# Performance work log

Measured on AMD Instinct MI355X. Metric: run time of the kernel, lower is better.

Reference implementation:

```python
import jax, jax.numpy as jnp
import numpy as np

HIDDEN = 2048
HEADS = 16
HEAD_DIM = HIDDEN // HEADS
ROPE_BASE = 10000.0


def rope_cos_sin(seq_len, dim, dtype=jnp.float32):
    inv_freq = 1.0 / (ROPE_BASE ** (jnp.arange(0, dim, 2, dtype=jnp.float32) / dim))
    t = jnp.arange(seq_len, dtype=jnp.float32)
    freqs = jnp.einsum('i,j->ij', t, inv_freq)            # [S, dim/2]
    emb = jnp.concatenate([freqs, freqs], axis=-1)        # [S, dim]
    return jnp.cos(emb).astype(dtype), jnp.sin(emb).astype(dtype)


def rotate_half(x):
    x1, x2 = jnp.split(x, 2, axis=-1)
    return jnp.concatenate([-x2, x1], axis=-1)


def setup_inputs() -> dict:
    key = jax.random.key(0)
    ks = jax.random.split(key, 6)
    B, S, D = 2, 2048, HIDDEN
    scale = 1.0 / np.sqrt(D)
    x = jax.random.normal(ks[0], (B, S, D), dtype=jnp.float32)
    Wq = jax.random.normal(ks[1], (D, D), dtype=jnp.float32) * scale
    Wk = jax.random.normal(ks[2], (D, D), dtype=jnp.float32) * scale
    Wv = jax.random.normal(ks[3], (D, D), dtype=jnp.float32) * scale
    Wo = jax.random.normal(ks[4], (D, D), dtype=jnp.float32) * scale
    bo = jnp.zeros((D,), dtype=jnp.float32)
    return {"x": x, "Wq": Wq, "Wk": Wk, "Wv": Wv, "Wo": Wo, "bo": bo}


def reference(x, Wq, Wk, Wv, Wo, bo):
    B, S, D = x.shape
    H, Dh = HEADS, HEAD_DIM
    # torch Linear: x @ W.T
    q = (x @ Wq.T).reshape(B, S, H, Dh).transpose(0, 2, 1, 3)  # [B,H,S,Dh]
    k = (x @ Wk.T).reshape(B, S, H, Dh).transpose(0, 2, 1, 3)
    v = (x @ Wv.T).reshape(B, S, H, Dh).transpose(0, 2, 1, 3)
    cos, sin = rope_cos_sin(S, Dh, x.dtype)                    # [S, Dh]
    q = q * cos + rotate_half(q) * sin
    k = k * cos + rotate_half(k) * sin
    scale = Dh ** -0.5
    attn = jnp.einsum('bhqd,bhkd->bhqk', q, k) * scale
    attn = jax.nn.softmax(attn, axis=-1)
    out = jnp.einsum('bhqk,bhkd->bhqd', attn, v)               # [B,H,S,Dh]
    out = out.transpose(0, 2, 1, 3).reshape(B, S, D)
    return out @ Wo.T + bo
```

## Files before the change

kernel.cpp:

```cpp
#include <hip/hip_runtime.h>
#include <stdint.h>


#define SEQ 2048
#define HD 128
#define DMODEL 2048

typedef __bf16 bf16x8 __attribute__((ext_vector_type(8)));
typedef float f32x4 __attribute__((ext_vector_type(4)));
typedef unsigned short u16;
typedef unsigned int u32;

typedef bf16x8 __attribute__((may_alias)) bf16x8_a;
typedef uint2 __attribute__((may_alias)) uint2_a;
typedef uint4 __attribute__((may_alias)) uint4_a;

__device__ __forceinline__ u16 f2bf(float f) {
  unsigned int u = __float_as_uint(f);
  u += 0x7fff + ((u >> 16) & 1);
  return (u16)(u >> 16);
}

typedef __attribute__((address_space(1))) void* gas_t;
typedef __attribute__((address_space(3))) void* las_t;
__device__ __forceinline__ void load_lds16(const void* g, void* l) {
  __builtin_amdgcn_global_load_lds((gas_t)(uintptr_t)g,
                                   (las_t)(uint32_t)(uintptr_t)l, 16, 0, 0);
}

__global__ void conv_all(const float* __restrict__ x,
                         const float* __restrict__ wq,
                         const float* __restrict__ wk,
                         const float* __restrict__ wv,
                         const float* __restrict__ wo,
                         u16* __restrict__ xb, u16* __restrict__ wqkv,
                         u16* __restrict__ wob) {
  int i = blockIdx.x * 256 + threadIdx.x;
  const float* src;
  u16* dst;
  int off;
  if (i < 2097152) { src = x; dst = xb; off = i; }
  else if (i < 3145728) { src = wq; dst = wqkv; off = i - 2097152; }
  else if (i < 4194304) { src = wk; dst = wqkv + 4194304; off = i - 3145728; }
  else if (i < 5242880) { src = wv; dst = wqkv + 8388608; off = i - 4194304; }
  else { src = wo; dst = wob; off = i - 5242880; }
  float4 v = ((const float4*)src)[off];
  ushort4 o;
  o.x = f2bf(v.x); o.y = f2bf(v.y); o.z = f2bf(v.z); o.w = f2bf(v.w);
  ((ushort4*)dst)[off] = o;
}


#define BARR asm volatile("s_barrier" ::: "memory")
#define LGKM0 asm volatile("s_waitcnt lgkmcnt(0)" ::: "memory")
#define VMW6 asm volatile("s_waitcnt vmcnt(6)" ::: "memory")
#define VMW8 asm volatile("s_waitcnt vmcnt(8)" ::: "memory")
#define VMW0 asm volatile("s_waitcnt vmcnt(0)" ::: "memory")

#define STGA(D, KOFF) do {                                                  \
    const u16* ga_ = Ag + (KOFF);                                           \
    u16* la_ = S + (D) * 16384;                                             \
    load_lds16(ga_ + off[0], la_ + tid * 8);                                \
    load_lds16(ga_ + off[1], la_ + (tid + 512) * 8);                        \
    load_lds16(ga_ + off[2], la_ + (tid + 1024) * 8);                       \
    load_lds16(ga_ + off[3], la_ + (tid + 1536) * 8);                       \
  } while (0)

#define STGB(D, KOFF) do {                                                  \
    const u16* gb_ = Bg + (KOFF);                                           \
    u16* lb_ = S + 49152 + (D) * 8192;                                      \
    load_lds16(gb_ + off[0], lb_ + tid * 8);                                \
    load_lds16(gb_ + off[1], lb_ + (tid + 512) * 8);                        \
  } while (0)

#define LDA2(D, MH) do {                                                    \
    const u16* ab_ = S + (D) * 16384;                                       \
    _Pragma("unroll") for (int mt_ = 0; mt_ < 2; ++mt_) {                   \
      int rA_ = wm * 64 + ((MH) * 2 + mt_) * 16 + l15;                      \
      int sw_ = rA_ & 7;                                                    \
      af[mt_][0] = *(const bf16x8_a*)(ab_ + (rA_ * 8 + (quad ^ sw_)) * 8);  \
      af[mt_][1] = *(const bf16x8_a*)(ab_ + (rA_ * 8 + ((4 + quad) ^ sw_)) * 8); \
    } } while (0)

#define LDB2(D) do {                                                        \
    const u16* bb_ = S + 49152 + (D) * 8192;                                \
    _Pragma("unroll") for (int nt_ = 0; nt_ < 4; ++nt_) {                   \
      int rB_ = wn * 64 + nt_ * 16 + l15;                                   \
      int sw_ = rB_ & 7;                                                    \
      bfr[nt_][0] = *(const bf16x8_a*)(bb_ + (rB_ * 8 + (quad ^ sw_)) * 8); \
      bfr[nt_][1] = *(const bf16x8_a*)(bb_ + (rB_ * 8 + ((4 + quad) ^ sw_)) * 8); \
    } } while (0)

#define MM2(MH) do {                                                        \
    __builtin_amdgcn_s_setprio(1);                                          \
    _Pragma("unroll") for (int c_ = 0; c_ < 2; ++c_)                        \
      _Pragma("unroll") for (int mt_ = 0; mt_ < 2; ++mt_)                   \
        _Pragma("unroll") for (int nt_ = 0; nt_ < 4; ++nt_) {               \
          if (VM)                                                           \
            acc[(MH) * 2 + mt_][nt_] =                                      \
                __builtin_amdgcn_mfma_f32_16x16x32_bf16(                    \
                    bfr[nt_][c_], af[mt_][c_],                              \
                    acc[(MH) * 2 + mt_][nt_], 0, 0, 0);                     \
          else                                                              \
            acc[(MH) * 2 + mt_][nt_] =                                      \
                __builtin_amdgcn_mfma_f32_16x16x32_bf16(                    \
                    af[mt_][c_], bfr[nt_][c_],                              \
                    acc[(MH) * 2 + mt_][nt_], 0, 0, 0);                     \
        }                                                                   \
    __builtin_amdgcn_s_setprio(0);                                          \
  } while (0)

#define STEP3(T, CUR, NX2) do {                                             \
    LDA2(CUR, 0); LDB2(CUR);                                                \
    STGA(NX2, ((T) + 2) * 64);                                              \
    BARR; LGKM0; MM2(0); BARR;                                              \
    LDA2(CUR, 1);                                                           \
    STGB(NX2, ((T) + 2) * 64);                                              \
    BARR; LGKM0; MM2(1); VMW6; BARR;                                        \
  } while (0)

template <bool VM>
__device__ __forceinline__ void mm_core(const u16* __restrict__ Ag,
                                        const u16* __restrict__ Bg,
                                        u16* __restrict__ S, int tid,
                                        f32x4 acc[4][4]) {
  const int lane = tid & 63;
  const int wave = tid >> 6;
  const int quad = lane >> 4;
  const int l15 = lane & 15;
  const int wm = wave >> 1;
  const int wn = wave & 1;

  u32 off[4];
#pragma unroll
  for (int j = 0; j < 4; ++j) {
    int idx = tid + j * 512;
    int r = idx >> 3;
    off[j] = (u32)r * 2048u + (u32)(((idx & 7) ^ (r & 7)) * 8);
  }

  bf16x8 af[2][2], bfr[4][2];

  STGA(0, 0);
  STGB(0, 0);
  STGA(1, 64);
  STGB(1, 64);
  VMW6;
  BARR;

#pragma unroll 1
  for (int tt = 0; tt < 30; tt += 3) {
    STEP3(tt,     0, 2);
    STEP3(tt + 1, 1, 0);
    STEP3(tt + 2, 2, 1);
  }

  LDA2(0, 0); LDB2(0);
  BARR; LGKM0; MM2(0); BARR;
  LDA2(0, 1);
  BARR; LGKM0; MM2(1); VMW0; BARR;
  LDA2(1, 0); LDB2(1);
  BARR; LGKM0; MM2(0); BARR;
  LDA2(1, 1);
  BARR; LGKM0; MM2(1); BARR;
}

__global__ __launch_bounds__(512, 2)
void gemm_qkv(const u16* __restrict__ A, const u16* __restrict__ Bm,
              u16* __restrict__ qkv, u16* __restrict__ vt) {
  __shared__ __align__(16) u16 S[73728];

  const int tid = threadIdx.x;
  int hwid = blockIdx.y * 48 + blockIdx.x;
  int logical = (hwid & 7) * 96 + (hwid >> 3);
  const int bx = logical >> 4;
  const int by = logical & 15;
  const int row0 = by * 256;
  const int col0 = bx * 128;
  const bool vmode = bx >= 32;

  const u16* Ag = A + (size_t)row0 * 2048;
  const u16* Bg = Bm + (size_t)col0 * 2048;

  f32x4 acc[4][4] = {};
  if (vmode) mm_core<true>(Ag, Bg, S, tid, acc);
  else       mm_core<false>(Ag, Bg, S, tid, acc);

  const int lane = tid & 63;
  const int wave = tid >> 6;
  const int quad = lane >> 4;
  const int l15 = lane & 15;
  const int wm = wave >> 1;
  const int wn = wave & 1;

  const int which = bx >> 4;
  const int h = bx & 15;
  const int brow = row0 >> 11;
  const int sbase = row0 & 2047;
  const float qs = (which == 0) ? 0.12751744f : 1.0f;

#pragma unroll
  for (int mt = 0; mt < 4; ++mt)
#pragma unroll
    for (int nt = 0; nt < 4; ++nt)
#pragma unroll
      for (int r = 0; r < 4; ++r) {
        int el;
        if (vmode) {
          int dd = wn * 64 + nt * 16 + quad * 4 + r;
          int ss = wm * 64 + mt * 16 + l15;
          el = dd * 256 + (((ss >> 3) ^ (dd & 31)) * 8) + (ss & 7);
        } else {
          int ss = wm * 64 + mt * 16 + quad * 4 + r;
          int dd = wn * 64 + nt * 16 + l15;
          el = ss * 128 + (((dd >> 3) ^ (ss & 15)) * 8) + (dd & 7);
        }
        S[el] = f2bf(acc[mt][nt][r] * qs);
      }
  __syncthreads();

  if (!vmode) {
    const int a = lane & 7;
    const int sg = lane >> 3;
    const float c1 = 0.2076205059304601f;
    const float c2 = 2.6514961294723187f;
#pragma unroll
    for (int pass = 0; pass < 4; ++pass) {
      int s_l = pass * 64 + wave * 8 + sg;
      int s2048 = sbase + s_l;
      int sw = s_l & 15;
      bf16x8 x1 = *(const bf16x8_a*)&S[s_l * 128 + ((a ^ sw) * 8)];
      bf16x8 x2 = *(const bf16x8_a*)&S[s_l * 128 + (((a + 8) ^ sw) * 8)];
      u16 o1[8], o2[8];
#pragma unroll
      for (int e = 0; e < 8; ++e) {
        float j = (float)(a * 8 + e);
        float rev = (float)s2048 * __builtin_amdgcn_exp2f(-c1 * j - c2);
        rev = __builtin_amdgcn_fractf(rev);
        float sn = __builtin_amdgcn_sinf(rev);
        float cs = __builtin_amdgcn_cosf(rev);
        float v1 = (float)x1[e], v2 = (float)x2[e];
        o1[e] = f2bf(v1 * cs - v2 * sn);
        o2[e] = f2bf(v2 * cs + v1 * sn);
      }
      size_t base =
          ((((size_t)which * 2 + brow) * 16 + h) * SEQ + s2048) * HD + a * 8;
      *(uint4_a*)&qkv[base] = *(uint4*)o1;
      *(uint4_a*)&qkv[base + 64] = *(uint4*)o2;
    }
  } else {
    const int d_part = tid >> 4;
    const int a0 = tid & 15;
#pragma unroll
    for (int pass = 0; pass < 4; ++pass) {
      int d_l = pass * 32 + d_part;
      int dw = d_l & 31;
      size_t rb = (((size_t)brow * 16 + h) * HD + d_l) * SEQ + sbase;
#pragma unroll
      for (int g = 0; g < 2; ++g) {
        int a2 = a0 + g * 16;
        bf16x8 y = *(const bf16x8_a*)&S[d_l * 256 + ((a2 ^ dw) * 8)];
        *(uint4_a*)&vt[rb + a2 * 8] = *(uint4_a*)&y;
      }
    }
  }
}

__global__ __launch_bounds__(512, 2)
void gemm_out(const u16* __restrict__ A, const u16* __restrict__ Bm,
              float* __restrict__ C, const float* __restrict__ bias) {
  __shared__ __align__(16) u16 S[73728];

  const int tid = threadIdx.x;
  int hwid = blockIdx.y * 16 + blockIdx.x;
  int logical = (hwid & 7) * 32 + (hwid >> 3);
  const int bx = logical >> 4;
  const int by = logical & 15;
  const int row0 = by * 256;
  const int col0 = bx * 128;

  const u16* Ag = A + (size_t)row0 * 2048;
  const u16* Bg = Bm + (size_t)col0 * 2048;

  f32x4 acc[4][4] = {};
  mm_core<false>(Ag, Bg, S, tid, acc);

  const int lane = tid & 63;
  const int wave = tid >> 6;
  const int quad = lane >> 4;
  const int l15 = lane & 15;
  const int wm = wave >> 1;
  const int wn = wave & 1;

#pragma unroll
  for (int nt = 0; nt < 4; ++nt) {
    int d = col0 + wn * 64 + nt * 16 + l15;
    float bv = bias[d];
#pragma unroll
    for (int mt = 0; mt < 4; ++mt) {
#pragma unroll
      for (int r = 0; r < 4; ++r) {
        int row = row0 + wm * 64 + mt * 16 + quad * 4 + r;
        C[(size_t)row * DMODEL + d] = acc[mt][nt][r] + bv;
      }
    }
  }
}

__global__ __launch_bounds__(256, 2)
void attn_kernel(const u16* __restrict__ qkv, const u16* __restrict__ vt,
                 u16* __restrict__ attn_out) {
  __shared__ __align__(16) u16 Kl[2][64 * 128];
  __shared__ __align__(16) u16 Vl[2][128 * 64];
  __shared__ __align__(16) u16 Pl[4][32 * 64];

  const int tid = threadIdx.x;
  const int lane = tid & 63;
  const int wave = tid >> 6;
  const int quad = lane >> 4;
  const int l15 = lane & 15;
  const int q0 = blockIdx.x * 128;
  const int bh = blockIdx.y;
  const size_t SD = (size_t)SEQ * HD;

  const u16* Q = qkv + (size_t)bh * SD;
  const u16* Kg = qkv + (size_t)(32 + bh) * SD;
  const u16* Vg = vt + (size_t)bh * SD;

  bf16x8 onesf;
#pragma unroll
  for (int e = 0; e < 8; ++e)
    onesf[e] = (l15 == 0) ? (__bf16)1.0f : (__bf16)0.0f;

  bf16x8 qf[2][4];
#pragma unroll
  for (int mt = 0; mt < 2; ++mt) {
    int qrow = q0 + wave * 32 + mt * 16 + l15;
#pragma unroll
    for (int c = 0; c < 4; ++c)
      qf[mt][c] = *(const bf16x8*)(Q + (size_t)qrow * HD + c * 32 + quad * 8);
  }

  f32x4 of[9][2] = {};
  u16* pw = &Pl[wave][0];

  auto stage = [&](int tile, int buf) {
    int kv0 = tile * 64;
#pragma unroll
    for (int j = 0; j < 4; ++j) {
      int idx = (wave * 4 + j) * 64 + lane;
      {
        int r = idx >> 4, cs = idx & 15;
        int cc = cs ^ (r & 15);
        load_lds16(Kg + (size_t)(kv0 + r) * HD + cc * 8, &Kl[buf][idx * 8]);
      }
      {
        int r = idx >> 3, cs = idx & 7;
        int cc = cs ^ (r & 7);
        load_lds16(Vg + (size_t)r * SEQ + kv0 + cc * 8, &Vl[buf][idx * 8]);
      }
    }
  };

  stage(0, 0);
  stage(1, 1);
  VMW8;
  BARR;

#pragma unroll 2
  for (int t = 0; t < 32; ++t) {
    const u16* Kb = Kl[t & 1];
    const u16* Vb = Vl[t & 1];

    f32x4 sc[4][2] = {};
    __builtin_amdgcn_s_setprio(1);
#pragma unroll
    for (int c = 0; c < 4; ++c) {
      bf16x8 kf[4];
#pragma unroll
      for (int nt = 0; nt < 4; ++nt)
        kf[nt] = *(const bf16x8*)&Kb[((nt * 16 + l15) * 16 +
                                      ((c * 4 + quad) ^ l15)) * 8];
#pragma unroll
      for (int nt = 0; nt < 4; ++nt)
#pragma unroll
        for (int mt = 0; mt < 2; ++mt)
          sc[nt][mt] = __builtin_amdgcn_mfma_f32_16x16x32_bf16(
              kf[nt], qf[mt][c], sc[nt][mt], 0, 0, 0);
    }
    __builtin_amdgcn_s_setprio(0);

#pragma unroll
    for (int nt = 0; nt < 4; ++nt) {
#pragma unroll
      for (int mt = 0; mt < 2; ++mt) {
        float p0 = __builtin_amdgcn_exp2f(sc[nt][mt][0]);
        float p1 = __builtin_amdgcn_exp2f(sc[nt][mt][1]);
        float p2 = __builtin_amdgcn_exp2f(sc[nt][mt][2]);
        float p3 = __builtin_amdgcn_exp2f(sc[nt][mt][3]);
        u32 lo = __builtin_amdgcn_perm(__float_as_uint(p1),
                                       __float_as_uint(p0), 0x07060302u);
        u32 hi = __builtin_amdgcn_perm(__float_as_uint(p3),
                                       __float_as_uint(p2), 0x07060302u);
        int row = mt * 16 + l15;
        int a = nt * 2 + (quad >> 1);
        int idx16 = (row * 8 + (a ^ (l15 & 7))) * 8 + (quad & 1) * 4;
        uint2 pk; pk.x = lo; pk.y = hi;
        *(uint2_a*)&pw[idx16] = pk;
      }
    }

    __builtin_amdgcn_s_setprio(1);
#pragma unroll
    for (int c = 0; c < 2; ++c) {
      bf16x8 pf[2];
#pragma unroll
      for (int mt = 0; mt < 2; ++mt)
        pf[mt] = *(const bf16x8_a*)&pw[((mt * 16 + l15) * 8 +
                                        ((c * 4 + quad) ^ (l15 & 7))) * 8];
#pragma unroll
      for (int dt = 0; dt < 9; ++dt) {
        bf16x8 vf = (dt < 8)
                        ? *(const bf16x8*)&Vb[((dt * 16 + l15) * 8 +
                                               ((c * 4 + quad) ^ (l15 & 7))) * 8]
                        : onesf;
#pragma unroll
        for (int mt = 0; mt < 2; ++mt)
          of[dt][mt] = __builtin_amdgcn_mfma_f32_16x16x32_bf16(
              vf, pf[mt], of[dt][mt], 0, 0, 0);
      }
    }
    __builtin_amdgcn_s_setprio(0);

    BARR;
    if (t < 30) {
      stage(t + 2, t & 1);
      VMW8;
    } else {
      VMW0;
    }
    BARR;
  }

  const int b = bh >> 4, h = bh & 15;
#pragma unroll
  for (int mt = 0; mt < 2; ++mt) {
    float lsum = __shfl(of[8][mt][0], l15, 64);
    float inv = 1.f / lsum;
    int s = q0 + wave * 32 + mt * 16 + l15;
    size_t rowb = ((size_t)b * SEQ + s) * DMODEL + h * HD;
#pragma unroll
    for (int dt = 0; dt < 8; ++dt) {
      ushort4 ov;
      ov.x = f2bf(of[dt][mt][0] * inv);
      ov.y = f2bf(of[dt][mt][1] * inv);
      ov.z = f2bf(of[dt][mt][2] * inv);
      ov.w = f2bf(of[dt][mt][3] * inv);
      *(ushort4*)&attn_out[rowb + dt * 16 + quad * 4] = ov;
    }
  }
}

extern "C" void kernel_launch(void* const* d_in, const int* in_sizes, int n_in,
                              void* d_out, int out_size, void* d_ws,
                              size_t ws_size, hipStream_t stream) {
  const float* x = (const float*)d_in[0];
  const float* Wq = (const float*)d_in[1];
  const float* Wk = (const float*)d_in[2];
  const float* Wv = (const float*)d_in[3];
  const float* Wo = (const float*)d_in[4];
  const float* bo = (const float*)d_in[5];
  float* out = (float*)d_out;

  char* ws = (char*)d_ws;
  u16* xb = (u16*)(ws);
  u16* wqkv = (u16*)(ws + (size_t)(16 << 20));
  u16* wob = (u16*)(ws + (size_t)(40 << 20));
  u16* qkv = (u16*)(ws + (size_t)(48 << 20));
  u16* vt = qkv + (size_t)2 * 8388608;
  u16* attn = xb;

  conv_all<<<24576, 256, 0, stream>>>(x, Wq, Wk, Wv, Wo, xb, wqkv, wob);

  gemm_qkv<<<dim3(48, 16), 512, 0, stream>>>(xb, wqkv, qkv, vt);
  attn_kernel<<<dim3(16, 32), 256, 0, stream>>>(qkv, vt, attn);
  gemm_out<<<dim3(16, 16), 512, 0, stream>>>(attn, wob, out, bo);
}
```

Measured before the change: 356.5 us.

## Remove intra-step barriers in GEMM core, coalesce output stores, batch conversion work

Removes the extra s_barrier and lgkmcnt waits around each MFMA half-step in the shared GEMM core, keeping only the per-step vmcnt wait and barrier that protect the async LDS staging. The output GEMM epilogue now adds bias in registers and stages the tile through LDS so rows are written with coalesced float4 stores. The fp32-to-bf16 conversion kernel processes four chunks per thread with a quarter of the grid. Dropping barriers relies on compiler-inserted waits for LDS reads and could expose races if buffer reuse assumptions are wrong.

After: 376.8 us. 5.7% more time.

```diff
diff --git a/kernel.cpp b/kernel.cpp
--- a/kernel.cpp
+++ b/kernel.cpp
@@ -14,6 +14,7 @@
 typedef bf16x8 __attribute__((may_alias)) bf16x8_a;
 typedef uint2 __attribute__((may_alias)) uint2_a;
 typedef uint4 __attribute__((may_alias)) uint4_a;
+typedef float4 __attribute__((may_alias)) float4_a;
 
 __device__ __forceinline__ u16 f2bf(float f) {
   unsigned int u = __float_as_uint(f);
@@ -35,24 +36,27 @@
                          const float* __restrict__ wo,
                          u16* __restrict__ xb, u16* __restrict__ wqkv,
                          u16* __restrict__ wob) {
-  int i = blockIdx.x * 256 + threadIdx.x;
-  const float* src;
-  u16* dst;
-  int off;
-  if (i < 2097152) { src = x; dst = xb; off = i; }
-  else if (i < 3145728) { src = wq; dst = wqkv; off = i - 2097152; }
-  else if (i < 4194304) { src = wk; dst = wqkv + 4194304; off = i - 3145728; }
-  else if (i < 5242880) { src = wv; dst = wqkv + 8388608; off = i - 4194304; }
-  else { src = wo; dst = wob; off = i - 5242880; }
-  float4 v = ((const float4*)src)[off];
-  ushort4 o;
-  o.x = f2bf(v.x); o.y = f2bf(v.y); o.z = f2bf(v.z); o.w = f2bf(v.w);
-  ((ushort4*)dst)[off] = o;
+  int base = blockIdx.x * 256 + threadIdx.x;
+#pragma unroll
+  for (int rep = 0; rep < 4; ++rep) {
+    int i = base + rep * 1572864;
+    const float* src;
+    u16* dst;
+    int off;
+    if (i < 2097152) { src = x; dst = xb; off = i; }
+    else if (i < 3145728) { src = wq; dst = wqkv; off = i - 2097152; }
+    else if (i < 4194304) { src = wk; dst = wqkv + 4194304; off = i - 3145728; }
+    else if (i < 5242880) { src = wv; dst = wqkv + 8388608; off = i - 4194304; }
+    else { src = wo; dst = wob; off = i - 5242880; }
+    float4 v = ((const float4*)src)[off];
+    ushort4 o;
+    o.x = f2bf(v.x); o.y = f2bf(v.y); o.z = f2bf(v.z); o.w = f2bf(v.w);
+    ((ushort4*)dst)[off] = o;
+  }
 }
 
 
 #define BARR asm volatile("s_barrier" ::: "memory")
-#define LGKM0 asm volatile("s_waitcnt lgkmcnt(0)" ::: "memory")
 #define VMW6 asm volatile("s_waitcnt vmcnt(6)" ::: "memory")
 #define VMW8 asm volatile("s_waitcnt vmcnt(8)" ::: "memory")
 #define VMW0 asm volatile("s_waitcnt vmcnt(0)" ::: "memory")
@@ -113,10 +117,11 @@
 #define STEP3(T, CUR, NX2) do {                                             \
     LDA2(CUR, 0); LDB2(CUR);                                                \
     STGA(NX2, ((T) + 2) * 64);                                              \
-    BARR; LGKM0; MM2(0); BARR;                                              \
+    MM2(0);                                                                 \
     LDA2(CUR, 1);                                                           \
     STGB(NX2, ((T) + 2) * 64);                                              \
-    BARR; LGKM0; MM2(1); VMW6; BARR;                                        \
+    MM2(1);                                                                 \
+    VMW6; BARR;                                                             \
   } while (0)
 
 template <bool VM>
@@ -156,13 +161,15 @@
   }
 
   LDA2(0, 0); LDB2(0);
-  BARR; LGKM0; MM2(0); BARR;
+  MM2(0);
   LDA2(0, 1);
-  BARR; LGKM0; MM2(1); VMW0; BARR;
+  MM2(1);
+  VMW0; BARR;
   LDA2(1, 0); LDB2(1);
-  BARR; LGKM0; MM2(0); BARR;
+  MM2(0);
   LDA2(1, 1);
-  BARR; LGKM0; MM2(1); BARR;
+  MM2(1);
+  BARR;
 }
 
 __global__ __launch_bounds__(512, 2)
@@ -294,16 +301,39 @@
 
 #pragma unroll
   for (int nt = 0; nt < 4; ++nt) {
-    int d = col0 + wn * 64 + nt * 16 + l15;
-    float bv = bias[d];
-#pragma unroll
-    for (int mt = 0; mt < 4; ++mt) {
-#pragma unroll
-      for (int r = 0; r < 4; ++r) {
-        int row = row0 + wm * 64 + mt * 16 + quad * 4 + r;
-        C[(size_t)row * DMODEL + d] = acc[mt][nt][r] + bv;
-      }
-    }
+    float bv = bias[col0 + wn * 64 + nt * 16 + l15];
+#pragma unroll
+    for (int mt = 0; mt < 4; ++mt)
+#pragma unroll
+      for (int r = 0; r < 4; ++r) acc[mt][nt][r] += bv;
+  }
+
+  float* Sf = (float*)S;
+  const int lr = tid >> 2;
+  const int c16 = (tid & 3) << 5;
+#pragma unroll
+  for (int hh = 0; hh < 2; ++hh) {
+    if ((wm >> 1) == hh) {
+      int lrow0 = (wm & 1) * 64;
+#pragma unroll
+      for (int mt = 0; mt < 4; ++mt)
+#pragma unroll
+        for (int nt = 0; nt < 4; ++nt)
+#pragma unroll
+          for (int r = 0; r < 4; ++r) {
+            int lrow = lrow0 + mt * 16 + quad * 4 + r;
+            int col = wn * 64 + nt * 16 + l15;
+            Sf[lrow * 132 + col] = acc[mt][nt][r];
+          }
+    }
+    __syncthreads();
+#pragma unroll
+    for (int k = 0; k < 8; ++k) {
+      float4 v = *(const float4_a*)&Sf[lr * 132 + c16 + k * 4];
+      *(float4_a*)&C[(size_t)(row0 + hh * 128 + lr) * DMODEL + col0 + c16 +
+                     k * 4] = v;
+    }
+    __syncthreads();
   }
 }
 
@@ -480,7 +510,7 @@
   u16* vt = qkv + (size_t)2 * 8388608;
   u16* attn = xb;
 
-  conv_all<<<24576, 256, 0, stream>>>(x, Wq, Wk, Wv, Wo, xb, wqkv, wob);
+  conv_all<<<6144, 256, 0, stream>>>(x, Wq, Wk, Wv, Wo, xb, wqkv, wob);
 
   gemm_qkv<<<dim3(48, 16), 512, 0, stream>>>(xb, wqkv, qkv, vt);
   attn_kernel<<<dim3(16, 32), 256, 0, stream>>>(qkv, vt, attn);
```

## Split attention work over 8 waves and drop redundant GEMM barriers

Applied to the files above, without the earlier changes.

The attention kernel now runs 512 threads per block, with each of the 8 waves owning 16 query rows instead of 32. This halves per-wave accumulators and registers and raises wave-level parallelism, at the cost of each wave reading K/V fragments from LDS for fewer rows. Separately, the GEMM main loop drops the extra s_barrier and lgkmcnt(0) waits around each MFMA half-step. It relies on the compiler's own waits and on multi-buffered staging to keep LDS reads safe, which reduces synchronisation stalls.

Measured after the change: 367.2 us. 1.03x slower.

```diff
diff --git a/kernel.cpp b/kernel.cpp
--- a/kernel.cpp
+++ b/kernel.cpp
@@ -52,9 +52,8 @@
 
 
 #define BARR asm volatile("s_barrier" ::: "memory")
-#define LGKM0 asm volatile("s_waitcnt lgkmcnt(0)" ::: "memory")
 #define VMW6 asm volatile("s_waitcnt vmcnt(6)" ::: "memory")
-#define VMW8 asm volatile("s_waitcnt vmcnt(8)" ::: "memory")
+#define VMW4 asm volatile("s_waitcnt vmcnt(4)" ::: "memory")
 #define VMW0 asm volatile("s_waitcnt vmcnt(0)" ::: "memory")
 
 #define STGA(D, KOFF) do {                                                  \
@@ -113,10 +112,11 @@
 #define STEP3(T, CUR, NX2) do {                                             \
     LDA2(CUR, 0); LDB2(CUR);                                                \
     STGA(NX2, ((T) + 2) * 64);                                              \
-    BARR; LGKM0; MM2(0); BARR;                                              \
+    MM2(0);                                                                 \
     LDA2(CUR, 1);                                                           \
     STGB(NX2, ((T) + 2) * 64);                                              \
-    BARR; LGKM0; MM2(1); VMW6; BARR;                                        \
+    MM2(1);                                                                 \
+    VMW6; BARR;                                                             \
   } while (0)
 
 template <bool VM>
@@ -156,13 +156,15 @@
   }
 
   LDA2(0, 0); LDB2(0);
-  BARR; LGKM0; MM2(0); BARR;
+  MM2(0);
   LDA2(0, 1);
-  BARR; LGKM0; MM2(1); VMW0; BARR;
+  MM2(1);
+  VMW0; BARR;
   LDA2(1, 0); LDB2(1);
-  BARR; LGKM0; MM2(0); BARR;
+  MM2(0);
   LDA2(1, 1);
-  BARR; LGKM0; MM2(1); BARR;
+  MM2(1);
+  BARR;
 }
 
 __global__ __launch_bounds__(512, 2)
@@ -307,12 +309,12 @@
   }
 }
 
-__global__ __launch_bounds__(256, 2)
+__global__ __launch_bounds__(512, 4)
 void attn_kernel(const u16* __restrict__ qkv, const u16* __restrict__ vt,
                  u16* __restrict__ attn_out) {
   __shared__ __align__(16) u16 Kl[2][64 * 128];
   __shared__ __align__(16) u16 Vl[2][128 * 64];
-  __shared__ __align__(16) u16 Pl[4][32 * 64];
+  __shared__ __align__(16) u16 Pl[8][16 * 64];
 
   const int tid = threadIdx.x;
   const int lane = tid & 63;
@@ -332,23 +334,22 @@
   for (int e = 0; e < 8; ++e)
     onesf[e] = (l15 == 0) ? (__bf16)1.0f : (__bf16)0.0f;
 
-  bf16x8 qf[2][4];
-#pragma unroll
-  for (int mt = 0; mt < 2; ++mt) {
-    int qrow = q0 + wave * 32 + mt * 16 + l15;
+  bf16x8 qf[4];
+  {
+    int qrow = q0 + wave * 16 + l15;
 #pragma unroll
     for (int c = 0; c < 4; ++c)
-      qf[mt][c] = *(const bf16x8*)(Q + (size_t)qrow * HD + c * 32 + quad * 8);
-  }
-
-  f32x4 of[9][2] = {};
+      qf[c] = *(const bf16x8*)(Q + (size_t)qrow * HD + c * 32 + quad * 8);
+  }
+
+  f32x4 of[9] = {};
   u16* pw = &Pl[wave][0];
 
   auto stage = [&](int tile, int buf) {
     int kv0 = tile * 64;
 #pragma unroll
-    for (int j = 0; j < 4; ++j) {
-      int idx = (wave * 4 + j) * 64 + lane;
+    for (int j = 0; j < 2; ++j) {
+      int idx = (wave * 2 + j) * 64 + lane;
       {
         int r = idx >> 4, cs = idx & 15;
         int cc = cs ^ (r & 15);
@@ -364,7 +365,7 @@
 
   stage(0, 0);
   stage(1, 1);
-  VMW8;
+  VMW4;
   BARR;
 
 #pragma unroll 2
@@ -372,7 +373,7 @@
     const u16* Kb = Kl[t & 1];
     const u16* Vb = Vl[t & 1];
 
-    f32x4 sc[4][2] = {};
+    f32x4 sc[4] = {};
     __builtin_amdgcn_s_setprio(1);
 #pragma unroll
     for (int c = 0; c < 4; ++c) {
@@ -383,51 +384,40 @@
                                       ((c * 4 + quad) ^ l15)) * 8];
 #pragma unroll
       for (int nt = 0; nt < 4; ++nt)
-#pragma unroll
-        for (int mt = 0; mt < 2; ++mt)
-          sc[nt][mt] = __builtin_amdgcn_mfma_f32_16x16x32_bf16(
-              kf[nt], qf[mt][c], sc[nt][mt], 0, 0, 0);
+        sc[nt] = __builtin_amdgcn_mfma_f32_16x16x32_bf16(
+            kf[nt], qf[c], sc[nt], 0, 0, 0);
     }
     __builtin_amdgcn_s_setprio(0);
 
 #pragma unroll
     for (int nt = 0; nt < 4; ++nt) {
-#pragma unroll
-      for (int mt = 0; mt < 2; ++mt) {
-        float p0 = __builtin_amdgcn_exp2f(sc[nt][mt][0]);
-        float p1 = __builtin_amdgcn_exp2f(sc[nt][mt][1]);
-        float p2 = __builtin_amdgcn_exp2f(sc[nt][mt][2]);
-        float p3 = __builtin_amdgcn_exp2f(sc[nt][mt][3]);
-        u32 lo = __builtin_amdgcn_perm(__float_as_uint(p1),
-                                       __float_as_uint(p0), 0x07060302u);
-        u32 hi = __builtin_amdgcn_perm(__float_as_uint(p3),
-                                       __float_as_uint(p2), 0x07060302u);
-        int row = mt * 16 + l15;
-        int a = nt * 2 + (quad >> 1);
-        int idx16 = (row * 8 + (a ^ (l15 & 7))) * 8 + (quad & 1) * 4;
-        uint2 pk; pk.x = lo; pk.y = hi;
-        *(uint2_a*)&pw[idx16] = pk;
-      }
+      float p0 = __builtin_amdgcn_exp2f(sc[nt][0]);
+      float p1 = __builtin_amdgcn_exp2f(sc[nt][1]);
+      float p2 = __builtin_amdgcn_exp2f(sc[nt][2]);
+      float p3 = __builtin_amdgcn_exp2f(sc[nt][3]);
+      u32 lo = __builtin_amdgcn_perm(__float_as_uint(p1),
+                                     __float_as_uint(p0), 0x07060302u);
+      u32 hi = __builtin_amdgcn_perm(__float_as_uint(p3),
+                                     __float_as_uint(p2), 0x07060302u);
+      int a = nt * 2 + (quad >> 1);
+      int idx16 = (l15 * 8 + (a ^ (l15 & 7))) * 8 + (quad & 1) * 4;
+      uint2 pk; pk.x = lo; pk.y = hi;
+      *(uint2_a*)&pw[idx16] = pk;
     }
 
     __builtin_amdgcn_s_setprio(1);
 #pragma unroll
     for (int c = 0; c < 2; ++c) {
-      bf16x8 pf[2];
-#pragma unroll
-      for (int mt = 0; mt < 2; ++mt)
-        pf[mt] = *(const bf16x8_a*)&pw[((mt * 16 + l15) * 8 +
-                                        ((c * 4 + quad) ^ (l15 & 7))) * 8];
+      bf16x8 pf = *(const bf16x8_a*)&pw[(l15 * 8 +
+                                         ((c * 4 + quad) ^ (l15 & 7))) * 8];
 #pragma unroll
       for (int dt = 0; dt < 9; ++dt) {
         bf16x8 vf = (dt < 8)
                         ? *(const bf16x8*)&Vb[((dt * 16 + l15) * 8 +
                                                ((c * 4 + quad) ^ (l15 & 7))) * 8]
                         : onesf;
-#pragma unroll
-        for (int mt = 0; mt < 2; ++mt)
-          of[dt][mt] = __builtin_amdgcn_mfma_f32_16x16x32_bf16(
-              vf, pf[mt], of[dt][mt], 0, 0, 0);
+        of[dt] = __builtin_amdgcn_mfma_f32_16x16x32_bf16(
+            vf, pf, of[dt], 0, 0, 0);
       }
     }
     __builtin_amdgcn_s_setprio(0);
@@ -435,7 +425,7 @@
     BARR;
     if (t < 30) {
       stage(t + 2, t & 1);
-      VMW8;
+      VMW4;
     } else {
       VMW0;
     }
@@ -443,19 +433,18 @@
   }
 
   const int b = bh >> 4, h = bh & 15;
-#pragma unroll
-  for (int mt = 0; mt < 2; ++mt) {
-    float lsum = __shfl(of[8][mt][0], l15, 64);
+  {
+    float lsum = __shfl(of[8][0], l15, 64);
     float inv = 1.f / lsum;
-    int s = q0 + wave * 32 + mt * 16 + l15;
+    int s = q0 + wave * 16 + l15;
     size_t rowb = ((size_t)b * SEQ + s) * DMODEL + h * HD;
 #pragma unroll
     for (int dt = 0; dt < 8; ++dt) {
       ushort4 ov;
-      ov.x = f2bf(of[dt][mt][0] * inv);
-      ov.y = f2bf(of[dt][mt][1] * inv);
-      ov.z = f2bf(of[dt][mt][2] * inv);
-      ov.w = f2bf(of[dt][mt][3] * inv);
+      ov.x = f2bf(of[dt][0] * inv);
+      ov.y = f2bf(of[dt][1] * inv);
+      ov.z = f2bf(of[dt][2] * inv);
+      ov.w = f2bf(of[dt][3] * inv);
       *(ushort4*)&attn_out[rowb + dt * 16 + quad * 4] = ov;
     }
   }
@@ -483,6 +472,6 @@
   conv_all<<<24576, 256, 0, stream>>>(x, Wq, Wk, Wv, Wo, xb, wqkv, wob);
 
   gemm_qkv<<<dim3(48, 16), 512, 0, stream>>>(xb, wqkv, qkv, vt);
-  attn_kernel<<<dim3(16, 32), 256, 0, stream>>>(qkv, vt, attn);
+  attn_kernel<<<dim3(16, 32), 512, 0, stream>>>(qkv, vt, attn);
   gemm_out<<<dim3(16, 16), 512, 0, stream>>>(attn, wob, out, bo);
 }
```
